# Kernel optimization log

Measured on AMD Instinct MI355X. Metric: run time of the kernel, lower is better.

Reference implementation:

```python
import jax, jax.numpy as jnp
import numpy as np

B, SM, SI, D, H, FF = 4, 1024, 4096, 256, 8, 1024
EPS = 1e-6

def _ln(x, g, b):
    m = jnp.mean(x, axis=-1, keepdims=True)
    v = jnp.mean(jnp.square(x - m), axis=-1, keepdims=True)
    return (x - m) * jax.lax.rsqrt(v + EPS) * g + b

def setup_inputs() -> dict:
    key = jax.random.key(0)
    ks = jax.random.split(key, 12)
    s = 0.02
    return {
        "state_seq": jax.random.normal(ks[0], (B, SM, D), jnp.float32),
        "input_seq": jax.random.normal(ks[1], (B, SI, D), jnp.float32),
        "Wk": jax.random.normal(ks[2], (D, D), jnp.float32) * s,
        "bk": jnp.zeros((D,), jnp.float32),
        "Wv": jax.random.normal(ks[3], (D, D), jnp.float32) * s,
        "bv": jnp.zeros((D,), jnp.float32),
        "Wq": jax.random.normal(ks[4], (H, D, D), jnp.float32) * s,
        "bq": jnp.zeros((H, D), jnp.float32),
        "Wo": jax.random.normal(ks[5], (H * D, D), jnp.float32) * s,
        "bo": jnp.zeros((D,), jnp.float32),
        "ln1_g": jnp.ones((D,), jnp.float32),
        "ln1_b": jnp.zeros((D,), jnp.float32),
        "W_in": jax.random.normal(ks[6], (D, FF), jnp.float32) * s,
        "b_in": jnp.zeros((FF,), jnp.float32),
        "Wg_nl": jax.random.normal(ks[7], (FF, FF), jnp.float32) * s,
        "bg_nl": jnp.zeros((FF,), jnp.float32),
        "Wg_l": jax.random.normal(ks[8], (FF, FF), jnp.float32) * s,
        "bg_l": jnp.zeros((FF,), jnp.float32),
        "Wg_o": jax.random.normal(ks[9], (FF, D), jnp.float32) * s,
        "bg_o": jnp.zeros((D,), jnp.float32),
        "ln2_g": jnp.ones((D,), jnp.float32),
        "ln2_b": jnp.zeros((D,), jnp.float32),
    }

def reference(state_seq, input_seq, Wk, bk, Wv, bv, Wq, bq, Wo, bo,
              ln1_g, ln1_b, W_in, b_in, Wg_nl, bg_nl, Wg_l, bg_l, Wg_o, bg_o,
              ln2_g, ln2_b):
    # shared key/value projections (multi-query: one K/V, many Q)
    ik = input_seq @ Wk + bk            # [B,SI,D]
    mk = state_seq @ Wk + bk            # [B,SM,D]
    iv = input_seq @ Wv + bv            # [B,SI,D]
    mv = state_seq @ Wv + bv            # [B,SM,D]
    # per-head queries from memory cells, stacked over H
    q = jnp.einsum('bmd,hde->hbme', state_seq, Wq) + bq[:, None, None, :]  # [H,B,SM,D]
    input_score = jnp.einsum('hbme,bse->hbms', q, ik)                      # [H,B,SM,SI]
    self_score = jnp.sum(q * mk[None], axis=-1, keepdims=True)             # [H,B,SM,1]
    score = jnp.concatenate([self_score, input_score], axis=-1)
    score = score / jnp.sqrt(jnp.asarray(D, score.dtype))
    attn = jax.nn.softmax(score, axis=-1)                                  # [H,B,SM,1+SI]
    val = jnp.einsum('hbms,bse->hbme', attn[..., 1:], iv) + attn[..., 0:1] * mv[None]
    concat = jnp.transpose(val, (1, 2, 0, 3)).reshape(val.shape[1], val.shape[2], -1)  # [B,SM,H*D]
    attn_out = concat @ Wo + bo
    x = _ln(attn_out + state_seq, ln1_g, ln1_b)
    h = jax.nn.relu(x @ W_in + b_in)                                       # [B,SM,FF]
    g = jax.nn.relu(h @ Wg_nl + bg_nl) * (h @ Wg_l + bg_l)
    ff = g @ Wg_o + bg_o
    return _ln(ff + x, ln2_g, ln2_b)
```

## Files before the change

### kernel.cpp

```cpp
#include <hip/hip_runtime.h>
#include <hip/hip_bf16.h>

typedef __bf16 bfx8 __attribute__((ext_vector_type(8)));
typedef __bf16 bfx4 __attribute__((ext_vector_type(4)));
typedef float  f32x4 __attribute__((ext_vector_type(4)));
typedef float  f32x16 __attribute__((ext_vector_type(16)));

#define MFMA16(a,b,c) __builtin_amdgcn_mfma_f32_16x16x32_bf16((a),(b),(c),0,0,0)
#define MFMA32(a,b,c) __builtin_amdgcn_mfma_f32_32x32x16_bf16((a),(b),(c),0,0,0)


#define PSCALE 0.09016844f
#define PCLAMP 43.2808512f

__device__ __forceinline__ unsigned cvtpk_bf16(float lo, float hi) {
  unsigned d;
  asm("v_cvt_pk_bf16_f32 %0, %1, %2" : "=v"(d) : "v"(lo), "v"(hi));
  return d;
}

__device__ __forceinline__ bfx8 packswap(const float* p) {
  unsigned a = cvtpk_bf16(p[0], p[1]);
  unsigned b = cvtpk_bf16(p[2], p[3]);
  unsigned c = cvtpk_bf16(p[4], p[5]);
  unsigned d = cvtpk_bf16(p[6], p[7]);
  asm("v_permlane32_swap_b32 %0, %1" : "+v"(a), "+v"(c));
  asm("v_permlane32_swap_b32 %0, %1" : "+v"(b), "+v"(d));
  union { unsigned u[4]; bfx8 v; } uu;
  uu.u[0] = a; uu.u[1] = b; uu.u[2] = c; uu.u[3] = d;
  return uu.v;
}

__device__ __forceinline__ void tile_tr(const float* __restrict__ src, __bf16* __restrict__ dst,
                                        int R, int C, int tile, float (*lt)[65]) {
  int tpr = C >> 6;
  int tr = tile / tpr, tc = tile % tpr;
  int c  = threadIdx.x & 63;
  int r0 = (threadIdx.x >> 6) << 4;
  const float* sp = src + (long)(tr * 64 + r0) * C + tc * 64 + c;
#pragma unroll
  for (int i = 0; i < 16; i++) lt[r0 + i][c] = sp[(long)i * C];
  __syncthreads();
  __bf16* dp = dst + (long)(tc * 64 + r0) * R + tr * 64 + c;
#pragma unroll
  for (int i = 0; i < 16; i++) dp[(long)i * R] = (__bf16)lt[c][r0 + i];
}

__global__ void trans_attn_t(const float* __restrict__ Wk, const float* __restrict__ Wv,
                             const float* __restrict__ Wq, const float* __restrict__ Wo,
                             __bf16* __restrict__ wkvqt, __bf16* __restrict__ wot) {
  __shared__ float lt[64][65];
  int t = blockIdx.x;
  if (t < 16)       tile_tr(Wk, wkvqt, 256, 256, t, lt);
  else if (t < 32)  tile_tr(Wv, wkvqt + 65536, 256, 256, t - 16, lt);
  else if (t < 160) {
    int e = t - 32, m = e >> 4;
    tile_tr(Wq + (long)m * 65536, wkvqt + 131072 + (long)m * 65536, 256, 256, e & 15, lt);
  } else            tile_tr(Wo, wot, 2048, 256, t - 160, lt);
}

__global__ void trans_ffn_t(const float* __restrict__ W_in, const float* __restrict__ Wg_nl,
                            const float* __restrict__ Wg_l, const float* __restrict__ Wg_o,
                            __bf16* __restrict__ dst) {
  __shared__ float lt[64][65];
  int t = blockIdx.x;
  if (t < 64)       tile_tr(W_in, dst, 256, 1024, t, lt);
  else if (t < 320) tile_tr(Wg_nl, dst + 262144, 1024, 1024, t - 64, lt);
  else if (t < 576) tile_tr(Wg_l, dst + 1310720, 1024, 1024, t - 320, lt);
  else              tile_tr(Wg_o, dst + 2359296, 1024, 256, t - 576, lt);
}

__device__ __forceinline__
void gemm_body(const __bf16* __restrict__ Xb, const float* __restrict__ Xf,
               const __bf16* __restrict__ Wt,
               const float* __restrict__ b1, const float* __restrict__ b2,
               const float* __restrict__ b3,
               __bf16* __restrict__ C, __bf16* __restrict__ C2, __bf16* __restrict__ C3,
               float* __restrict__ Cf,
               int M, int N, int Kfull, int kspan, int xmode, int mode, int act,
               int bx, int by, int bz, __bf16* xs, __bf16* wsm) {
  const int tid  = threadIdx.x;
  const int lane = tid & 63;
  const int w    = tid >> 6;
  const int l15  = lane & 15;
  const int quad = lane >> 4;
  const int wm   = (w >> 1) * 64;
  const int wn   = (w & 1) * 64;
  const int m0   = bx * 128;
  const int n0   = by * 128;
  const int k0   = (mode == 7) ? bz * kspan : 0;

  f32x4 acc[4][4];
#pragma unroll
  for (int i = 0; i < 4; i++)
#pragma unroll
    for (int j = 0; j < 4; j++) acc[i][j] = (f32x4){0.f, 0.f, 0.f, 0.f};

  for (int kk = k0; kk < k0 + kspan; kk += 64) {
    __syncthreads();
#pragma unroll
    for (int rep = 0; rep < 4; rep++) {
      int idx = rep * 256 + tid;
      int row = idx >> 3;
      int g   = idx & 7;
      if (xmode == 1) {
        const float* p = Xf + (long)(m0 + row) * Kfull + kk + g * 8;
        f32x4 a0 = *(const f32x4*)p;
        f32x4 a1 = *(const f32x4*)(p + 4);
        bfx8 v;
#pragma unroll
        for (int j = 0; j < 4; j++) { v[j] = (__bf16)a0[j]; v[4 + j] = (__bf16)a1[j]; }
        *(bfx8*)&xs[row * 72 + g * 8] = v;
      } else if (xmode == 2) {
        const __bf16* p = Xb + (long)(m0 + row) * 2048 + kk + g * 8;
        bfx8 a = *(const bfx8*)p;
        bfx8 bb = *(const bfx8*)(p + 1024);
        bfx8 v;
#pragma unroll
        for (int j = 0; j < 8; j++) v[j] = (__bf16)((float)a[j] * (float)bb[j]);
        *(bfx8*)&xs[row * 72 + g * 8] = v;
      } else {
        *(bfx8*)&xs[row * 72 + g * 8] = *(const bfx8*)(Xb + (long)(m0 + row) * Kfull + kk + g * 8);
      }
      *(bfx8*)&wsm[row * 72 + g * 8] = *(const bfx8*)(Wt + (long)(n0 + row) * Kfull + kk + g * 8);
    }
    __syncthreads();
#pragma unroll
    for (int ks = 0; ks < 2; ks++) {
      bfx8 af[4], bf_[4];
#pragma unroll
      for (int i = 0; i < 4; i++) af[i]  = *(const bfx8*)&xs[(wm + 16 * i + l15) * 72 + ks * 32 + quad * 8];
#pragma unroll
      for (int j = 0; j < 4; j++) bf_[j] = *(const bfx8*)&wsm[(wn + 16 * j + l15) * 72 + ks * 32 + quad * 8];
#pragma unroll
      for (int i = 0; i < 4; i++)
#pragma unroll
        for (int j = 0; j < 4; j++) acc[i][j] = MFMA16(af[i], bf_[j], acc[i][j]);
    }
  }

#pragma unroll
  for (int j = 0; j < 4; j++) {
    int n = n0 + wn + 16 * j + l15;
    float bv;
    if (mode == 4)      bv = (n < 256) ? b1[n] : b2[n - 256];
    else if (mode == 5) bv = (n < 256) ? b1[n] : (n < 512) ? b2[n - 256] : b3[n - 512];
    else if (mode == 6) bv = (n < 1024) ? b1[n] : b2[n - 1024];
    else if (mode == 7) bv = (bz == 0) ? b1[n] : 0.f;
    else                bv = b1[n];
#pragma unroll
    for (int i = 0; i < 4; i++) {
#pragma unroll
      for (int r = 0; r < 4; r++) {
        int m = m0 + wm + 16 * i + quad * 4 + r;
        float v = acc[i][j][r] + bv;
        if (mode == 6) { if (n < 1024) v = fmaxf(v, 0.f); }
        else if (act == 1) v = fmaxf(v, 0.f);
        if (mode == 4) {
          if (n < 256) C[(long)m * 256 + n] = (__bf16)v;
          else {
            int bb_ = m >> 12, si = m & 4095;
            C2[((long)(bb_ * 128 + (si >> 5)) * 256 + (n - 256)) * 32 + (si & 31)] = (__bf16)v;
          }
        } else if (mode == 5) {
          if (n < 256)      C[(long)m * 256 + n] = (__bf16)v;
          else if (n < 512) C2[(long)m * 256 + (n - 256)] = (__bf16)v;
          else {
            int nn = n - 512, hhh = nn >> 8, dd = nn & 255;
            C3[(long)hhh * 1048576 + (long)m * 256 + dd] = (__bf16)v;
          }
        } else if (mode == 7) {
          Cf[(long)bz * M * N + (long)m * N + n] = v;
        } else {
          C[(long)m * N + n] = (__bf16)v;
        }
      }
    }
  }
}

__global__ __launch_bounds__(256)
void gemm_bt(const __bf16* Xb, const float* Xf, const __bf16* Wt,
             const float* b1, const float* b2, const float* b3,
             __bf16* C, __bf16* C2, __bf16* C3, float* Cf,
             int M, int N, int Kfull, int kspan, int xmode, int mode, int act) {
  __shared__ __bf16 xs[128 * 72];
  __shared__ __bf16 wsm[128 * 72];
  gemm_body(Xb, Xf, Wt, b1, b2, b3, C, C2, C3, Cf, M, N, Kfull, kspan, xmode, mode, act,
            blockIdx.x, blockIdx.y, blockIdx.z, xs, wsm);
}

__global__ __launch_bounds__(256)
void proj2(const float* input, const float* state, const __bf16* Wkvqt,
           const float* bk, const float* bv, const float* bq,
           __bf16* ik, __bf16* ivT, __bf16* mk, __bf16* mv, __bf16* qbuf) {
  __shared__ __bf16 xs[128 * 72];
  __shared__ __bf16 wsm[128 * 72];
  int bid = blockIdx.x;
  if (bid < 512) {
    gemm_body(nullptr, input, Wkvqt, bk, bv, nullptr, ik, ivT, nullptr, nullptr,
              16384, 512, 256, 256, 1, 4, 0, bid & 127, bid >> 7, 0, xs, wsm);
  } else {
    int b2 = bid - 512;
    gemm_body(nullptr, state, Wkvqt, bk, bv, bq, mk, mv, qbuf, nullptr,
              4096, 2560, 256, 256, 1, 5, 0, b2 & 31, b2 >> 5, 0, xs, wsm);
  }
}

__global__ __launch_bounds__(256)
void attn_kernel(const __bf16* __restrict__ qb,
                 const __bf16* __restrict__ ik,
                 const __bf16* __restrict__ ivT,
                 const __bf16* __restrict__ mk,
                 const __bf16* __restrict__ mv,
                 __bf16* __restrict__ concat) {
  __shared__ __bf16 lk[2][32][264];
  __shared__ __bf16 lvt[2][256][40];

  const int tid  = threadIdx.x;
  const int lane = tid & 63;
  const int w    = tid >> 6;
  const int l31  = lane & 31;
  const int h    = lane >> 5;

  const int m0 = blockIdx.x * 128;
  const int b  = blockIdx.y;
  const int hh = blockIdx.z;
  const int mw = m0 + w * 32;

  const long qbase  = ((long)hh * 4096 + b * 1024 + mw) * 256;
  const long kvbase = (long)b * 4096 * 256;
  const long vtbase = (long)b * 128 * 8192;
  const long mbase  = ((long)b * 1024 + mw) * 256;

  bfx8 qf[16];
  {
    const __bf16* qrow = qb + qbase + (long)l31 * 256 + h * 8;
#pragma unroll
    for (int kt = 0; kt < 16; kt++) qf[kt] = *(const bfx8*)(qrow + kt * 16);
  }

  float ps_l;
  {
    const __bf16* krow = mk + mbase + (long)l31 * 256 + h * 8;
    float s = 0.f;
#pragma unroll
    for (int kt = 0; kt < 16; kt++) {
      bfx8 kv = *(const bfx8*)(krow + kt * 16);
#pragma unroll
      for (int j = 0; j < 8; j++) s += (float)qf[kt][j] * (float)kv[j];
    }
    s += __shfl_xor(s, 32);
    ps_l = __builtin_amdgcn_exp2f(fminf(s * PSCALE, PCLAMP));
  }

  f32x16 oacc[8];
#pragma unroll
  for (int dt = 0; dt < 8; dt++)
#pragma unroll
    for (int i = 0; i < 16; i++) oacc[dt][i] = 0.f;
  float den_l = 0.f;
  bfx8 pf0c, pf1c;

  f32x16 zz;
#pragma unroll
  for (int i = 0; i < 16; i++) zz[i] = 0.f;

  auto sload_k = [&](int c, bfx8* kreg) {
    const long kb = kvbase + (long)c * 8192;
#pragma unroll
    for (int rep = 0; rep < 4; rep++) {
      int idx = rep * 256 + tid;
      kreg[rep] = *(const bfx8*)(ik + kb + (long)(idx >> 5) * 256 + (idx & 31) * 8);
    }
  };
  auto sload_v = [&](int c, bfx8* vreg) {
    const long vb = vtbase + (long)c * 8192;
#pragma unroll
    for (int rep = 0; rep < 4; rep++) {
      int idx = rep * 256 + tid;
      vreg[rep] = *(const bfx8*)(ivT + vb + (long)idx * 8);
    }
  };
  auto sstore_k = [&](int slot, const bfx8* kreg) {
#pragma unroll
    for (int rep = 0; rep < 4; rep++) {
      int idx = rep * 256 + tid;
      *(bfx8*)&lk[slot][idx >> 5][(idx & 31) * 8] = kreg[rep];
    }
  };
  auto sstore_v = [&](int slot, const bfx8* vreg) {
#pragma unroll
    for (int rep = 0; rep < 4; rep++) {
      int idx = rep * 256 + tid;
      *(bfx8*)&lvt[slot][idx >> 2][(idx & 3) * 8] = vreg[rep];
    }
  };

  auto chunkMFMA = [&](int vslot, int kslot, bool doS, bool doPV, f32x16* sa) {
#pragma unroll
    for (int t = 0; t < 8; t++) {
      bfx8 vf0, vf1, kf0, kf1;
      if (doPV) {
        vf0 = *(const bfx8*)&lvt[vslot][t * 32 + l31][h * 8];
        vf1 = *(const bfx8*)&lvt[vslot][t * 32 + l31][16 + h * 8];
      }
      if (doS) {
        kf0 = *(const bfx8*)&lk[kslot][l31][(2 * t) * 16 + h * 8];
        kf1 = *(const bfx8*)&lk[kslot][l31][(2 * t + 1) * 16 + h * 8];
      }
      if (doPV) oacc[t] = MFMA32(pf0c, vf0, oacc[t]);
      if (doS) {
        if (t < 2) sa[2 * t] = MFMA32(kf0, qf[2 * t], zz);
        else       sa[(2 * t) & 3] = MFMA32(kf0, qf[2 * t], sa[(2 * t) & 3]);
      }
      if (doPV) oacc[t] = MFMA32(pf1c, vf1, oacc[t]);
      if (doS) {
        if (t < 2) sa[2 * t + 1] = MFMA32(kf1, qf[2 * t + 1], zz);
        else       sa[(2 * t + 1) & 3] = MFMA32(kf1, qf[2 * t + 1], sa[(2 * t + 1) & 3]);
      }
    }
  };

  auto finishP = [&](const f32x16* sa) {
    float p[16];
#pragma unroll
    for (int r = 0; r < 16; r++) {
      float s = (sa[0][r] + sa[1][r]) + (sa[2][r] + sa[3][r]);
      p[r] = __builtin_amdgcn_exp2f(fminf(s * PSCALE, PCLAMP));
      den_l += p[r];
    }
    pf0c = packswap(p);
    pf1c = packswap(p + 8);
  };

  {
    bfx8 kreg[4], vreg[4];
    sload_k(0, kreg);
    sload_v(0, vreg);
    sstore_k(0, kreg);
    sstore_v(0, vreg);
    sload_k(1, kreg);
    sstore_k(1, kreg);
  }
  __syncthreads();

  f32x16 sa[4];
  chunkMFMA(0, 0, true, false, sa);
  finishP(sa);
  __syncthreads();

  for (int i = 0; i < 126; i++) {
    bfx8 kreg[4], vreg[4];
    sload_k(i + 2, kreg);
    sload_v(i + 1, vreg);
    chunkMFMA(i & 1, (i + 1) & 1, true, true, sa);
    sstore_k(i & 1, kreg);
    sstore_v((i + 1) & 1, vreg);
    finishP(sa);
    __syncthreads();
  }
  {
    bfx8 vreg[4];
    sload_v(127, vreg);
    chunkMFMA(0, 1, true, true, sa);
    sstore_v(1, vreg);
    finishP(sa);
    __syncthreads();
  }
  chunkMFMA(1, 0, false, true, sa);

  float tot = den_l + __shfl_xor(den_l, 32) + ps_l;
#pragma unroll
  for (int r = 0; r < 16; r++) {
    int row = (r & 3) + 8 * (r >> 2) + 4 * h;
    float ps   = __shfl(ps_l, row);
    float dinv = 1.f / __shfl(tot, row);
    const __bf16* mvrow = mv + mbase + (long)row * 256;
    __bf16* crow = concat + ((long)(b * 1024 + mw + row)) * 2048 + hh * 256;
#pragma unroll
    for (int dt = 0; dt < 8; dt++) {
      int d = dt * 32 + l31;
      crow[d] = (__bf16)((oacc[dt][r] + ps * (float)mvrow[d]) * dinv);
    }
  }
}

__global__ __launch_bounds__(256)
void ln4_kernel(const float* __restrict__ parts, const float* __restrict__ res,
                const float* __restrict__ g, const float* __restrict__ beta,
                __bf16* __restrict__ outb, float* __restrict__ outf) {
  int row  = blockIdx.x * 4 + (threadIdx.x >> 6);
  int lane = threadIdx.x & 63;
  const float* p = parts + (long)row * 256 + lane * 4;
  f32x4 a0 = *(const f32x4*)p;
  f32x4 a1 = *(const f32x4*)(p + 1048576);
  f32x4 a2 = *(const f32x4*)(p + 2097152);
  f32x4 a3 = *(const f32x4*)(p + 3145728);
  f32x4 rv = *(const f32x4*)(res + (long)row * 256 + lane * 4);
  float v[4], s1 = 0.f, s2 = 0.f;
#pragma unroll
  for (int i = 0; i < 4; i++) {
    v[i] = a0[i] + a1[i] + a2[i] + a3[i] + rv[i];
    s1 += v[i];
    s2 += v[i] * v[i];
  }
#pragma unroll
  for (int off = 32; off >= 1; off >>= 1) {
    s1 += __shfl_xor(s1, off);
    s2 += __shfl_xor(s2, off);
  }
  float mean = s1 * (1.f / 256.f);
  float var  = fmaxf(s2 * (1.f / 256.f) - mean * mean, 0.f);
  float rstd = rsqrtf(var + 1e-6f);
#pragma unroll
  for (int i = 0; i < 4; i++) {
    int c = lane * 4 + i;
    float o = (v[i] - mean) * rstd * g[c] + beta[c];
    if (outb) outb[(long)row * 256 + c] = (__bf16)o;
    if (outf) outf[(long)row * 256 + c] = o;
  }
}

extern "C" void kernel_launch(void* const* d_in, const int* in_sizes, int n_in,
                              void* d_out, int out_size, void* d_ws, size_t ws_size,
                              hipStream_t stream) {
  const float* state  = (const float*)d_in[0];
  const float* input  = (const float*)d_in[1];
  const float* Wk     = (const float*)d_in[2];
  const float* bk     = (const float*)d_in[3];
  const float* Wv     = (const float*)d_in[4];
  const float* bv     = (const float*)d_in[5];
  const float* Wq     = (const float*)d_in[6];
  const float* bq     = (const float*)d_in[7];
  const float* Wo     = (const float*)d_in[8];
  const float* bo     = (const float*)d_in[9];
  const float* ln1g   = (const float*)d_in[10];
  const float* ln1b   = (const float*)d_in[11];
  const float* W_in   = (const float*)d_in[12];
  const float* b_in   = (const float*)d_in[13];
  const float* Wg_nl  = (const float*)d_in[14];
  const float* bg_nl  = (const float*)d_in[15];
  const float* Wg_l   = (const float*)d_in[16];
  const float* bg_l   = (const float*)d_in[17];
  const float* Wg_o   = (const float*)d_in[18];
  const float* bg_o   = (const float*)d_in[19];
  const float* ln2g   = (const float*)d_in[20];
  const float* ln2b   = (const float*)d_in[21];
  float* out = (float*)d_out;

  const size_t needed_elems = 28442624;
  if (ws_size < needed_elems * sizeof(__bf16)) return;

  __bf16* ws = (__bf16*)d_ws;
  size_t off = 0;
  auto alloc = [&](size_t n) { __bf16* p = ws + off; off += n; return p; };
  __bf16* Wkvqt  = alloc(655360);
  __bf16* Wot    = alloc(524288);
  __bf16* ik     = alloc(4194304);
  __bf16* ivT    = alloc(4194304);
  __bf16* mk     = alloc(1048576);
  __bf16* mv     = alloc(1048576);
  __bf16* qbuf   = alloc(8388608);
  __bf16* concat = alloc(8388608);
  float*  wo_parts = (float*)qbuf;
  __bf16* x      = mv;
  __bf16* hbuf   = ik;
  __bf16* t12    = qbuf;
  float*  ff_parts = (float*)ik;
  __bf16* Wffn   = concat;
  float*  xf     = (float*)(concat + 3670016);

  dim3 blk(256);

  trans_attn_t<<<dim3(288), blk, 0, stream>>>(Wk, Wv, Wq, Wo, Wkvqt, Wot);

  proj2<<<dim3(1152), blk, 0, stream>>>(input, state, Wkvqt, bk, bv, bq,
                                        ik, ivT, mk, mv, qbuf);

  attn_kernel<<<dim3(8, 4, 8), blk, 0, stream>>>(qbuf, ik, ivT, mk, mv, concat);

  gemm_bt<<<dim3(32, 2, 4), blk, 0, stream>>>(concat, nullptr, Wot, bo, nullptr, nullptr,
                                              nullptr, nullptr, nullptr, wo_parts,
                                              4096, 256, 2048, 512, 0, 7, 0);
  ln4_kernel<<<dim3(1024), blk, 0, stream>>>(wo_parts, state, ln1g, ln1b, x, xf);

  trans_ffn_t<<<dim3(640), blk, 0, stream>>>(W_in, Wg_nl, Wg_l, Wg_o, Wffn);

  gemm_bt<<<dim3(32, 8), blk, 0, stream>>>(x, nullptr, Wffn, b_in, nullptr, nullptr,
                                           hbuf, nullptr, nullptr, nullptr,
                                           4096, 1024, 256, 256, 0, 0, 1);
  gemm_bt<<<dim3(32, 16), blk, 0, stream>>>(hbuf, nullptr, Wffn + 262144, bg_nl, bg_l, nullptr,
                                            t12, nullptr, nullptr, nullptr,
                                            4096, 2048, 1024, 1024, 0, 6, 0);
  gemm_bt<<<dim3(32, 2, 4), blk, 0, stream>>>(t12, nullptr, Wffn + 2359296, bg_o, nullptr, nullptr,
                                              nullptr, nullptr, nullptr, ff_parts,
                                              4096, 256, 1024, 256, 2, 7, 0);
  ln4_kernel<<<dim3(1024), blk, 0, stream>>>(ff_parts, xf, ln2g, ln2b, nullptr, out);
}
```

Before: 458.2 us.

## Split attention key range across two wave groups per block with LDS reduction

The attention kernel now launches 512 threads per block, and the two halves each process half of the 4096 input keys (64 chunks each) for the same 128 query rows. Partial output accumulators and denominators from the second half go through LDS, are summed into the first half, and the first half writes the final result. This doubles the active waves per query tile, since the original grid of 256 blocks underfills the GPU. In exchange it adds a cross-half reduction through LDS, doubles shared memory per block and puts more register pressure on each block.

```diff
diff --git a/kernel.cpp b/kernel.cpp
--- a/kernel.cpp
+++ b/kernel.cpp
@@ -207,26 +207,35 @@
   }
 }
 
-__global__ __launch_bounds__(256)
+__global__ __launch_bounds__(512, 2)
 void attn_kernel(const __bf16* __restrict__ qb,
                  const __bf16* __restrict__ ik,
                  const __bf16* __restrict__ ivT,
                  const __bf16* __restrict__ mk,
                  const __bf16* __restrict__ mv,
                  __bf16* __restrict__ concat) {
-  __shared__ __bf16 lk[2][32][264];
-  __shared__ __bf16 lvt[2][256][40];
+  __shared__ union {
+    struct {
+      __bf16 lk[2][2][32][264];
+      __bf16 lvt[2][2][256][40];
+    } s;
+    float ex[4 * 8192 + 128];
+  } sm;
 
   const int tid  = threadIdx.x;
   const int lane = tid & 63;
   const int w    = tid >> 6;
+  const int half = w >> 2;
+  const int wq   = w & 3;
+  const int t256 = tid & 255;
   const int l31  = lane & 31;
   const int h    = lane >> 5;
 
   const int m0 = blockIdx.x * 128;
   const int b  = blockIdx.y;
   const int hh = blockIdx.z;
-  const int mw = m0 + w * 32;
+  const int mw = m0 + wq * 32;
+  const int c0 = half * 64;
 
   const long qbase  = ((long)hh * 4096 + b * 1024 + mw) * 256;
   const long kvbase = (long)b * 4096 * 256;
@@ -270,7 +279,7 @@
     const long kb = kvbase + (long)c * 8192;
 #pragma unroll
     for (int rep = 0; rep < 4; rep++) {
-      int idx = rep * 256 + tid;
+      int idx = rep * 256 + t256;
       kreg[rep] = *(const bfx8*)(ik + kb + (long)(idx >> 5) * 256 + (idx & 31) * 8);
     }
   };
@@ -278,22 +287,22 @@
     const long vb = vtbase + (long)c * 8192;
 #pragma unroll
     for (int rep = 0; rep < 4; rep++) {
-      int idx = rep * 256 + tid;
+      int idx = rep * 256 + t256;
       vreg[rep] = *(const bfx8*)(ivT + vb + (long)idx * 8);
     }
   };
   auto sstore_k = [&](int slot, const bfx8* kreg) {
 #pragma unroll
     for (int rep = 0; rep < 4; rep++) {
-      int idx = rep * 256 + tid;
-      *(bfx8*)&lk[slot][idx >> 5][(idx & 31) * 8] = kreg[rep];
+      int idx = rep * 256 + t256;
+      *(bfx8*)&sm.s.lk[half][slot][idx >> 5][(idx & 31) * 8] = kreg[rep];
     }
   };
   auto sstore_v = [&](int slot, const bfx8* vreg) {
 #pragma unroll
     for (int rep = 0; rep < 4; rep++) {
-      int idx = rep * 256 + tid;
-      *(bfx8*)&lvt[slot][idx >> 2][(idx & 3) * 8] = vreg[rep];
+      int idx = rep * 256 + t256;
+      *(bfx8*)&sm.s.lvt[half][slot][idx >> 2][(idx & 3) * 8] = vreg[rep];
     }
   };
 
@@ -302,12 +311,12 @@
     for (int t = 0; t < 8; t++) {
       bfx8 vf0, vf1, kf0, kf1;
       if (doPV) {
-        vf0 = *(const bfx8*)&lvt[vslot][t * 32 + l31][h * 8];
-        vf1 = *(const bfx8*)&lvt[vslot][t * 32 + l31][16 + h * 8];
+        vf0 = *(const bfx8*)&sm.s.lvt[half][vslot][t * 32 + l31][h * 8];
+        vf1 = *(const bfx8*)&sm.s.lvt[half][vslot][t * 32 + l31][16 + h * 8];
       }
       if (doS) {
-        kf0 = *(const bfx8*)&lk[kslot][l31][(2 * t) * 16 + h * 8];
-        kf1 = *(const bfx8*)&lk[kslot][l31][(2 * t + 1) * 16 + h * 8];
+        kf0 = *(const bfx8*)&sm.s.lk[half][kslot][l31][(2 * t) * 16 + h * 8];
+        kf1 = *(const bfx8*)&sm.s.lk[half][kslot][l31][(2 * t + 1) * 16 + h * 8];
       }
       if (doPV) oacc[t] = MFMA32(pf0c, vf0, oacc[t]);
       if (doS) {
@@ -336,11 +345,11 @@
 
   {
     bfx8 kreg[4], vreg[4];
-    sload_k(0, kreg);
-    sload_v(0, vreg);
+    sload_k(c0, kreg);
+    sload_v(c0, vreg);
     sstore_k(0, kreg);
     sstore_v(0, vreg);
-    sload_k(1, kreg);
+    sload_k(c0 + 1, kreg);
     sstore_k(1, kreg);
   }
   __syncthreads();
@@ -350,10 +359,10 @@
   finishP(sa);
   __syncthreads();
 
-  for (int i = 0; i < 126; i++) {
+  for (int i = 0; i < 62; i++) {
     bfx8 kreg[4], vreg[4];
-    sload_k(i + 2, kreg);
-    sload_v(i + 1, vreg);
+    sload_k(c0 + i + 2, kreg);
+    sload_v(c0 + i + 1, vreg);
     chunkMFMA(i & 1, (i + 1) & 1, true, true, sa);
     sstore_k(i & 1, kreg);
     sstore_v((i + 1) & 1, vreg);
@@ -362,26 +371,54 @@
   }
   {
     bfx8 vreg[4];
-    sload_v(127, vreg);
+    sload_v(c0 + 63, vreg);
     chunkMFMA(0, 1, true, true, sa);
     sstore_v(1, vreg);
     finishP(sa);
     __syncthreads();
   }
   chunkMFMA(1, 0, false, true, sa);
-
-  float tot = den_l + __shfl_xor(den_l, 32) + ps_l;
-#pragma unroll
-  for (int r = 0; r < 16; r++) {
-    int row = (r & 3) + 8 * (r >> 2) + 4 * h;
-    float ps   = __shfl(ps_l, row);
-    float dinv = 1.f / __shfl(tot, row);
-    const __bf16* mvrow = mv + mbase + (long)row * 256;
-    __bf16* crow = concat + ((long)(b * 1024 + mw + row)) * 2048 + hh * 256;
-#pragma unroll
-    for (int dt = 0; dt < 8; dt++) {
-      int d = dt * 32 + l31;
-      crow[d] = (__bf16)((oacc[dt][r] + ps * (float)mvrow[d]) * dinv);
+  __syncthreads();
+
+  float den_row = den_l + __shfl_xor(den_l, 32);
+  if (half == 1) {
+    float* eo = sm.ex + wq * 8192;
+#pragma unroll
+    for (int dt = 0; dt < 8; dt++)
+#pragma unroll
+      for (int rq = 0; rq < 4; rq++) {
+        f32x4 v4 = { oacc[dt][rq * 4 + 0], oacc[dt][rq * 4 + 1],
+                     oacc[dt][rq * 4 + 2], oacc[dt][rq * 4 + 3] };
+        *(f32x4*)&eo[(dt * 4 + rq) * 256 + lane * 4] = v4;
+      }
+    if (h == 0) sm.ex[4 * 8192 + wq * 32 + l31] = den_row;
+  }
+  __syncthreads();
+  if (half == 0) {
+    const float* eo = sm.ex + wq * 8192;
+#pragma unroll
+    for (int dt = 0; dt < 8; dt++)
+#pragma unroll
+      for (int rq = 0; rq < 4; rq++) {
+        f32x4 v4 = *(const f32x4*)&eo[(dt * 4 + rq) * 256 + lane * 4];
+#pragma unroll
+        for (int j = 0; j < 4; j++) oacc[dt][rq * 4 + j] += v4[j];
+      }
+    float den1 = sm.ex[4 * 8192 + wq * 32 + l31];
+    float tot  = den_row + den1 + ps_l;
+
+#pragma unroll
+    for (int r = 0; r < 16; r++) {
+      int row = (r & 3) + 8 * (r >> 2) + 4 * h;
+      float ps   = __shfl(ps_l, row);
+      float dinv = 1.f / __shfl(tot, row);
+      const __bf16* mvrow = mv + mbase + (long)row * 256;
+      __bf16* crow = concat + ((long)(b * 1024 + mw + row)) * 2048 + hh * 256;
+#pragma unroll
+      for (int dt = 0; dt < 8; dt++) {
+        int d = dt * 32 + l31;
+        crow[d] = (__bf16)((oacc[dt][r] + ps * (float)mvrow[d]) * dinv);
+      }
     }
   }
 }
@@ -478,7 +515,7 @@
   proj2<<<dim3(1152), blk, 0, stream>>>(input, state, Wkvqt, bk, bv, bq,
                                         ik, ivT, mk, mv, qbuf);
 
-  attn_kernel<<<dim3(8, 4, 8), blk, 0, stream>>>(qbuf, ik, ivT, mk, mv, concat);
+  attn_kernel<<<dim3(8, 4, 8), dim3(512), 0, stream>>>(qbuf, ik, ivT, mk, mv, concat);
 
   gemm_bt<<<dim3(32, 2, 4), blk, 0, stream>>>(concat, nullptr, Wot, bo, nullptr, nullptr,
                                               nullptr, nullptr, nullptr, wo_parts,
```

After: 639.5 us. 39.6% more time.
